# Kernel tuning notes

Hardware: AMD Instinct MI355X
Metric: run time of the kernel (lower is better)

## Reference

```python
import jax, jax.numpy as jnp
import numpy as np

B, S, D_IN, D_OUT, H = 4, 2048, 1024, 1024, 16
HD = D_OUT // H  # 64


def setup_inputs() -> dict:
    key = jax.random.key(0)
    ks = jax.random.split(key, 6)
    s = 1.0 / np.sqrt(D_IN)
    return {
        "x": jax.random.normal(ks[0], (B, S, D_IN), dtype=jnp.float32),
        "Wq": jax.random.uniform(ks[1], (D_IN, D_OUT), jnp.float32, -s, s),
        "Wk": jax.random.uniform(ks[2], (D_IN, D_OUT), jnp.float32, -s, s),
        "Wv": jax.random.uniform(ks[3], (D_IN, D_OUT), jnp.float32, -s, s),
        "Wo": jax.random.uniform(ks[4], (D_OUT, D_OUT), jnp.float32, -s, s),
        "bo": jax.random.uniform(ks[5], (D_OUT,), jnp.float32, -s, s),
    }


def reference(x, Wq, Wk, Wv, Wo, bo):
    b, s, _ = x.shape
    # QKV projections -> [b, H, s, hd]
    def split_heads(t):
        return t.reshape(b, s, H, HD).transpose(0, 2, 1, 3)
    q = split_heads(x @ Wq)
    k = split_heads(x @ Wk)
    v = split_heads(x @ Wv)
    # attention scores [b, H, s, s]
    scores = jnp.einsum("bhqd,bhkd->bhqk", q, k)
    causal = jnp.triu(jnp.ones((s, s), dtype=bool), k=1)
    scores = jnp.where(causal, -jnp.inf, scores)
    attn = jax.nn.softmax(scores / np.sqrt(HD), axis=-1)
    ctx = jnp.einsum("bhqk,bhkd->bhqd", attn, v)
    ctx = ctx.transpose(0, 2, 1, 3).reshape(b, s, D_OUT)
    return ctx @ Wo + bo
```

## Files before the change

kernel.cpp:

```cpp
#include <hip/hip_runtime.h>

typedef __attribute__((ext_vector_type(8))) short bf16x8;
typedef __attribute__((ext_vector_type(4))) float f32x4;
typedef __attribute__((ext_vector_type(4))) unsigned uint4v;

#define SM_C 0.18033688011112042f
#define MFMA16 __builtin_amdgcn_mfma_f32_16x16x32_bf16

__device__ __forceinline__ unsigned short f2bf(float f) {
  unsigned u = __builtin_bit_cast(unsigned, f);
  u += 0x7fffu + ((u >> 16) & 1u);
  return (unsigned short)(u >> 16);
}

__device__ __forceinline__ unsigned cvtpk(float lo, float hi) {
  unsigned r;
  asm volatile("v_cvt_pk_bf16_f32 %0, %1, %2" : "=v"(r) : "v"(lo), "v"(hi));
  return r;
}

__device__ __forceinline__ void gload16(const void* g, void* lds) {
  __builtin_amdgcn_global_load_lds(
      (const __attribute__((address_space(1))) void*)g,
      (__attribute__((address_space(3))) void*)lds, 16, 0, 0);
}

#define BARRIER __builtin_amdgcn_s_barrier()
#define ABARRIER asm volatile("s_barrier" ::: "memory")
#define LGKM0 asm volatile("s_waitcnt lgkmcnt(0)" ::: "memory")

__global__ __launch_bounds__(256) void cvt_x(const float* __restrict__ in,
                                             unsigned short* __restrict__ out,
                                             int n4) {
  int i = blockIdx.x * 256 + threadIdx.x;
  int stride = gridDim.x * 256;
  for (; i < n4; i += stride) {
    float4 v = ((const float4*)in)[i];
    unsigned short o0 = f2bf(v.x), o1 = f2bf(v.y), o2 = f2bf(v.z), o3 = f2bf(v.w);
    unsigned long long packed = (unsigned long long)o0 | ((unsigned long long)o1 << 16) |
                                ((unsigned long long)o2 << 32) | ((unsigned long long)o3 << 48);
    ((unsigned long long*)out)[i] = packed;
  }
}

__global__ __launch_bounds__(256) void transpose_w4(const float* __restrict__ W0,
                                                    const float* __restrict__ W1,
                                                    const float* __restrict__ W2,
                                                    const float* __restrict__ W3,
                                                    unsigned short* __restrict__ WT) {
  __shared__ float tile[32][33];
  const int z = blockIdx.z;
  const float* W = (z == 0) ? W0 : (z == 1) ? W1 : (z == 2) ? W2 : W3;
  unsigned short* WTo = WT + (size_t)z * 1048576;
  int bx = blockIdx.x, by = blockIdx.y;
  int x = bx * 32 + threadIdx.x;
  for (int i = 0; i < 4; ++i) {
    int r = threadIdx.y + i * 8;
    tile[r][threadIdx.x] = W[(by * 32 + r) * 1024 + x];
  }
  __syncthreads();
  int nx = by * 32 + threadIdx.x;
  for (int i = 0; i < 4; ++i) {
    int r = threadIdx.y + i * 8;
    WTo[(long)(bx * 32 + r) * 1024 + nx] = f2bf(tile[threadIdx.x][r]);
  }
}

__global__ __launch_bounds__(256) void transpose_v(const unsigned short* __restrict__ QKV,
                                                   unsigned short* __restrict__ Vt) {
  __shared__ alignas(16) unsigned short tile[64][74];
  const int bid = blockIdx.x;
  const int st = bid & 31, bh = bid >> 5;
  const int b = bh >> 4, h = bh & 15;
  const int t = threadIdx.x;
  const int r = t >> 2, c16 = (t & 3) * 16;
  const unsigned short* src =
      QKV + ((long)(b * 2048 + st * 64 + r)) * 3072 + 2048 + h * 64 + c16;
  uint4v v0 = *(const uint4v*)src;
  uint4v v1 = *(const uint4v*)(src + 8);
  unsigned* dst32 = (unsigned*)&tile[r][c16];
  dst32[0] = v0[0]; dst32[1] = v0[1]; dst32[2] = v0[2]; dst32[3] = v0[3];
  dst32[4] = v1[0]; dst32[5] = v1[1]; dst32[6] = v1[2]; dst32[7] = v1[3];
  __syncthreads();
  const int lw = t & 63, w = t >> 6;
  const int vp = (lw & 32) | (((lw >> 2) & 3) << 3) | (((lw >> 4) & 1) << 2) | (lw & 3);
#pragma unroll
  for (int k = 0; k < 16; ++k) {
    int hd = w * 16 + k;
    Vt[((long)(bh * 64 + hd)) * 2048 + st * 64 + vp] = tile[lw][hd];
  }
}

template <int NR, int FP32OUT>
__global__ __launch_bounds__(512, 1) void gemm3b(const unsigned short* __restrict__ A,
                                                 const unsigned short* __restrict__ BT,
                                                 unsigned short* __restrict__ Cb,
                                                 float* __restrict__ Cf,
                                                 const float* __restrict__ bias,
                                                 int M, int N, int K) {
  constexpr int BN = NR * 64;
  __shared__ alignas(16) unsigned short As[3][256 * 64];
  __shared__ alignas(16) unsigned short Bs[2][BN * 64];

  const int nbn = N / BN;
  const int tmg = (M / 256) / 8;
  const int cc = blockIdx.x >> 3, xc = blockIdx.x & 7;
  const int tm = xc * tmg + cc / nbn, tn = cc % nbn;

  const int t = threadIdx.x, l = t & 63, wid = t >> 6;
  const int wm = wid >> 2, wn = wid & 3;
  const int lr = l & 15, lg = l >> 4;

  f32x4 acc[8][NR] = {};

  const int sq = t >> 3;
  const int sslot8 = ((t & 7) ^ (sq & 7)) * 8;
  const unsigned short* Ath = A + ((long)tm * 256 + sq) * K + sslot8;
  const unsigned short* Bth = BT + ((long)tn * BN + sq) * K + sslot8;
  const int ldsoff = sq * 64 + (t & 7) * 8;

#define STGA(buf, q, kt) \
  gload16(Ath + (long)((q)*64) * K + (kt)*64, &As[buf][(q)*4096 + ldsoff])
#define STGB(buf, u, kt) \
  gload16(Bth + (long)((u)*64) * K + (kt)*64, &Bs[buf][(u)*4096 + ldsoff])

  const int NT = K >> 6;
#pragma unroll
  for (int q = 0; q < 4; ++q) STGA(0, q, 0);
#pragma unroll
  for (int u = 0; u < NR; ++u) STGB(0, u, 0);
#pragma unroll
  for (int q = 0; q < 4; ++q) STGA(1, q, 1);

  const int offk0 = (lg ^ (lr & 7)) * 8;
  const int offk1 = ((4 + lg) ^ (lr & 7)) * 8;
  const int arow0 = (wm * 128 + lr) * 64;
  const int brow0 = (wn * (NR * 16) + lr) * 64;

#define DS_A(MH)                                                   \
  _Pragma("unroll") for (int m_ = 0; m_ < 4; ++m_) {               \
    const unsigned short* ap_ = Ac + arow0 + ((MH)*4 + m_) * 1024; \
    af[m_][0] = *(const bf16x8*)(ap_ + offk0);                     \
    af[m_][1] = *(const bf16x8*)(ap_ + offk1);                     \
  }
#define DS_B_ALL                                          \
  _Pragma("unroll") for (int n_ = 0; n_ < NR; ++n_) {     \
    const unsigned short* bp_ = Bc + brow0 + n_ * 1024;   \
    bfr[n_][0] = *(const bf16x8*)(bp_ + offk0);           \
    bfr[n_][1] = *(const bf16x8*)(bp_ + offk1);           \
  }
#define MM(MH)                                                              \
  __builtin_amdgcn_s_setprio(1);                                            \
  _Pragma("unroll") for (int m_ = 0; m_ < 4; ++m_)                          \
  _Pragma("unroll") for (int n_ = 0; n_ < NR; ++n_) {                       \
    acc[(MH)*4 + m_][n_] = MFMA16(af[m_][0], bfr[n_][0],                    \
                                  acc[(MH)*4 + m_][n_], 0, 0, 0);           \
    acc[(MH)*4 + m_][n_] = MFMA16(af[m_][1], bfr[n_][1],                    \
                                  acc[(MH)*4 + m_][n_], 0, 0, 0);           \
  }                                                                         \
  __builtin_amdgcn_s_setprio(0);

  int cur3 = 0;
  int stg3 = 2;
  for (int tt = 0; tt < NT; ++tt) {
    const unsigned short* Ac = As[cur3];
    const unsigned short* Bc = Bs[tt & 1];

    bf16x8 af[4][2];
    bf16x8 bfr[NR][2];

    if (tt == NT - 1) asm volatile("s_waitcnt vmcnt(0)" ::: "memory");
    else              asm volatile("s_waitcnt vmcnt(4)" ::: "memory");
    BARRIER;
    DS_A(0);
    DS_B_ALL;
    if (tt + 1 < NT) {
      const int nbB = (tt + 1) & 1;
#pragma unroll
      for (int u = 0; u < NR; ++u) STGB(nbB, u, tt + 1);
    }
    BARRIER;
    LGKM0;
    MM(0);

    DS_A(1);
    if (tt + 2 < NT) {
#pragma unroll
      for (int q = 0; q < 4; ++q) STGA(stg3, q, tt + 2);
    }
    BARRIER;
    LGKM0;
    MM(1);

    cur3 = (cur3 == 2) ? 0 : cur3 + 1;
    stg3 = (stg3 == 2) ? 0 : stg3 + 1;
  }
#undef DS_A
#undef DS_B_ALL
#undef MM
#undef STGA
#undef STGB

  const long crow = (long)tm * 256 + wm * 128;
  const int ccol = tn * BN + wn * (NR * 16);
#pragma unroll
  for (int m = 0; m < 8; ++m)
#pragma unroll
    for (int n = 0; n < NR; ++n)
#pragma unroll
      for (int r = 0; r < 4; ++r) {
        long row = crow + m * 16 + lg * 4 + r;
        int col = ccol + n * 16 + lr;
        if (FP32OUT)
          Cf[row * N + col] = acc[m][n][r] + bias[col];
        else
          Cb[row * N + col] = f2bf(acc[m][n][r]);
      }
}

template <int TWO>
__device__ __forceinline__ void attn_tile(
    const unsigned short* __restrict__ Kc, const unsigned short* __restrict__ Vc,
    int lr, int lg, bool mask0, bool mask1, int kv0, int q0row, int q1row,
    const bf16x8 (&qf)[2][2], f32x4 (&cacc)[2][4], float (&m_r)[2], float (&l_r)[2]) {
  constexpr int S0 = TWO ? 0 : 1;
  f32x4 p[2][4];
#pragma unroll
  for (int s = S0; s < 2; ++s)
#pragma unroll
    for (int g = 0; g < 4; ++g) p[s][g] = f32x4{0.f, 0.f, 0.f, 0.f};

  __builtin_amdgcn_s_setprio(1);
#pragma unroll
  for (int g = 0; g < 4; ++g) {
    const int key = g * 16 + lr;
    const int swz = (key & 7) << 3;
#pragma unroll
    for (int c = 0; c < 2; ++c) {
      bf16x8 kf = *(const bf16x8*)(Kc + key * 64 + ((c * 32 + lg * 8) ^ swz));
#pragma unroll
      for (int s = S0; s < 2; ++s)
        p[s][g] = MFMA16(kf, qf[s][c], p[s][g], 0, 0, 0);
    }
  }
  __builtin_amdgcn_s_setprio(0);

  if (TWO && mask0) {
#pragma unroll
    for (int g = 0; g < 4; ++g)
#pragma unroll
      for (int r = 0; r < 4; ++r)
        if (kv0 + g * 16 + lg * 4 + r > q0row) p[0][g][r] = -1e30f;
  }
  if (mask1) {
#pragma unroll
    for (int g = 0; g < 4; ++g)
#pragma unroll
      for (int r = 0; r < 4; ++r)
        if (kv0 + g * 16 + lg * 4 + r > q1row) p[1][g][r] = -1e30f;
  }

  unsigned pk[2][4][2];
#pragma unroll
  for (int s = S0; s < 2; ++s) {
    float mloc = p[s][0][0];
#pragma unroll
    for (int g = 0; g < 4; ++g)
#pragma unroll
      for (int r = 0; r < 4; ++r) mloc = fmaxf(mloc, p[s][g][r]);
    mloc = fmaxf(mloc, __shfl_xor(mloc, 16));
    mloc = fmaxf(mloc, __shfl_xor(mloc, 32));
    const bool defer = __all(mloc <= m_r[s] + 44.0f);
    const float mn = defer ? m_r[s] : fmaxf(m_r[s], mloc);
    const float nmc = -mn * SM_C;
    float rs = 0.f;
#pragma unroll
    for (int g = 0; g < 4; ++g)
#pragma unroll
      for (int r = 0; r < 4; ++r) {
        float e = __builtin_amdgcn_exp2f(__builtin_fmaf(p[s][g][r], SM_C, nmc));
        p[s][g][r] = e;
        rs += e;
      }
    rs += __shfl_xor(rs, 16);
    rs += __shfl_xor(rs, 32);
    if (defer) {
      l_r[s] += rs;
    } else {
      float alpha = __builtin_amdgcn_exp2f((m_r[s] - mn) * SM_C);
      l_r[s] = l_r[s] * alpha + rs;
      m_r[s] = mn;
      float alq[4];
#pragma unroll
      for (int r = 0; r < 4; ++r) alq[r] = __shfl(alpha, lg * 20 + r);
#pragma unroll
      for (int n = 0; n < 4; ++n)
#pragma unroll
        for (int r = 0; r < 4; ++r) cacc[s][n][r] *= alq[r];
    }
#pragma unroll
    for (int g = 0; g < 4; ++g) {
      pk[s][g][0] = cvtpk(p[s][g][0], p[s][g][1]);
      pk[s][g][1] = cvtpk(p[s][g][2], p[s][g][3]);
    }
  }

#pragma unroll
  for (int sl = 0; sl < 2; ++sl) {
    bf16x8 vf[4];
#pragma unroll
    for (int n = 0; n < 4; ++n) {
      const int hd = n * 16 + lr;
      vf[n] = *(const bf16x8*)(Vc + hd * 64 + ((sl * 32 + lg * 8) ^ ((hd & 7) << 3)));
    }
    __builtin_amdgcn_s_setprio(1);
#pragma unroll
    for (int s = S0; s < 2; ++s) {
      uint4v pw = {pk[s][2 * sl][0], pk[s][2 * sl][1], pk[s][2 * sl + 1][0], pk[s][2 * sl + 1][1]};
      bf16x8 pa = __builtin_bit_cast(bf16x8, pw);
#pragma unroll
      for (int n = 0; n < 4; ++n)
        cacc[s][n] = MFMA16(pa, vf[n], cacc[s][n], 0, 0, 0);
    }
    __builtin_amdgcn_s_setprio(0);
  }
}

__global__ __launch_bounds__(256, 4) void flash_attn(const unsigned short* __restrict__ QKV,
                                                     const unsigned short* __restrict__ Vt,
                                                     unsigned short* __restrict__ Ctx) {
  __shared__ alignas(16) unsigned short Ks[2][64 * 64];
  __shared__ alignas(16) unsigned short Vs[2][64 * 64];
  const int bid = blockIdx.x;
  const int qt = bid >> 6;
  const int bh = bid & 63;
  const int b = bh >> 4, h = bh & 15;
  const int t = threadIdx.x, l = t & 63, w = t >> 6;
  const int lr = l & 15, lg = l >> 4;
  const long rowbase = (long)b * 2048;
  const int colbase = h * 64;
  const int q0 = qt * 64 + w * 16;
  const int q1 = (31 - qt) * 64 + w * 16;
  const int q0row = q0 + lr, q1row = q1 + lr;
  const int nkv = 32 - qt;

  bf16x8 qf[2][2];
#pragma unroll
  for (int c = 0; c < 2; ++c) {
    qf[0][c] = *(const bf16x8*)(QKV + (rowbase + q0 + lr) * 3072 + colbase + c * 32 + lg * 8);
    qf[1][c] = *(const bf16x8*)(QKV + (rowbase + q1 + lr) * 3072 + colbase + c * 32 + lg * 8);
  }

  f32x4 cacc[2][4];
  float m_r[2], l_r[2];
#pragma unroll
  for (int s = 0; s < 2; ++s) {
    m_r[s] = -1e30f;
    l_r[s] = 0.f;
#pragma unroll
    for (int n = 0; n < 4; ++n) cacc[s][n] = f32x4{0.f, 0.f, 0.f, 0.f};
  }

  const int srow = w * 16 + (l >> 3);
  const int scol = (l & 7) * 8;
  const int kswz = scol ^ ((srow & 7) << 3);
  const unsigned short* kp = QKV + (rowbase + srow) * 3072 + 1024 + colbase + kswz;
  const unsigned short* vp = Vt + ((long)(bh * 64 + srow)) * 2048 + kswz;
  unsigned short* ksd0 = &Ks[0][(w * 16) * 64];
  unsigned short* vsd0 = &Vs[0][(w * 16) * 64];

#define STAGE(buf)                                    \
  do {                                                \
    gload16(kp, ksd0 + (buf) * 4096);                 \
    gload16(kp + 8 * 3072, ksd0 + (buf) * 4096 + 512);\
    gload16(vp, vsd0 + (buf) * 4096);                 \
    gload16(vp + 8 * 2048, vsd0 + (buf) * 4096 + 512);\
    kp += 64 * 3072;                                  \
    vp += 64;                                         \
  } while (0)

#define TILE_WAIT(j)                                                          \
  do {                                                                        \
    if ((j) == nkv - 1) asm volatile("s_waitcnt vmcnt(0)" ::: "memory");      \
    else                asm volatile("s_waitcnt vmcnt(4)" ::: "memory");      \
    asm volatile("s_barrier" ::: "memory");                                   \
  } while (0)

  STAGE(0);
  STAGE(1);

  int j = 0;
  for (; j <= qt; ++j) {
    const int cur = j & 1;
    TILE_WAIT(j);
    attn_tile<1>(Ks[cur], Vs[cur], lr, lg, j == qt, false, j * 64, q0row, q1row,
                 qf, cacc, m_r, l_r);
    asm volatile("s_barrier" ::: "memory");
    if (j + 2 < nkv) STAGE(cur);
  }
  for (; j < nkv; ++j) {
    const int cur = j & 1;
    TILE_WAIT(j);
    attn_tile<0>(Ks[cur], Vs[cur], lr, lg, false, j == nkv - 1, j * 64, q0row, q1row,
                 qf, cacc, m_r, l_r);
    asm volatile("s_barrier" ::: "memory");
    if (j + 2 < nkv) STAGE(cur);
  }
#undef STAGE
#undef TILE_WAIT

#pragma unroll
  for (int s = 0; s < 2; ++s) {
    float invl = 1.f / l_r[s];
    float ilq[4];
#pragma unroll
    for (int r = 0; r < 4; ++r) ilq[r] = __shfl(invl, lg * 20 + r);
    const int qs = (s == 0) ? q0 : q1;
#pragma unroll
    for (int n = 0; n < 4; ++n)
#pragma unroll
      for (int r = 0; r < 4; ++r) {
        long row = rowbase + qs + lg * 4 + r;
        Ctx[row * 1024 + colbase + n * 16 + lr] = f2bf(cacc[s][n][r] * ilq[r]);
      }
  }
}

extern "C" void kernel_launch(void* const* d_in, const int* in_sizes, int n_in,
                              void* d_out, int out_size, void* d_ws, size_t ws_size,
                              hipStream_t stream) {
  (void)in_sizes; (void)n_in; (void)out_size; (void)ws_size;
  const float* x  = (const float*)d_in[0];
  const float* Wq = (const float*)d_in[1];
  const float* Wk = (const float*)d_in[2];
  const float* Wv = (const float*)d_in[3];
  const float* Wo = (const float*)d_in[4];
  const float* bo = (const float*)d_in[5];
  float* out = (float*)d_out;

  unsigned short* ws = (unsigned short*)d_ws;
  unsigned short* xb  = ws;
  unsigned short* Vt  = ws;
  unsigned short* WqT = ws + 8388608;
  unsigned short* WkT = WqT + 1048576;
  unsigned short* WvT = WkT + 1048576;
  unsigned short* WoT = WvT + 1048576;
  unsigned short* QKV = WoT + 1048576;
  unsigned short* Ctx = QKV + 25165824;

  cvt_x<<<2048, 256, 0, stream>>>(x, xb, 8192 * 1024 / 4);

  dim3 tb(32, 8), tg(32, 32, 4);
  transpose_w4<<<tg, tb, 0, stream>>>(Wq, Wk, Wv, Wo, WqT);

  gemm3b<3, 0><<<512, 512, 0, stream>>>(xb, WqT, QKV, nullptr, nullptr,
                                        8192, 3072, 1024);

  transpose_v<<<2048, 256, 0, stream>>>(QKV, Vt);

  flash_attn<<<1024, 256, 0, stream>>>(QKV, Vt, Ctx);

  gemm3b<2, 1><<<256, 512, 0, stream>>>(Ctx, WoT, nullptr, out, bo,
                                        8192, 1024, 1024);
}
```

Measured before the change: 159.3 us.

## Fuse V transpose into QKV GEMM epilogue and pack softmax math

The QKV GEMM epilogue now writes Q and K into separate contiguous planes and writes V directly in the permuted transposed layout used by attention. This removes the separate transpose_v kernel and its extra read and write of V. The GEMM tile width is reduced from NR=3 to NR=2 with more blocks so that each tile column maps onto exactly one plane. The attention softmax is also rewritten to use packed fp32 FMA, add and mul instructions. The V epilogue now issues scattered 8-byte stores, and the smaller tile lowers per-block reuse in the GEMM.

```diff
diff --git a/kernel.cpp b/kernel.cpp
--- a/kernel.cpp
+++ b/kernel.cpp
@@ -2,6 +2,7 @@
 
 typedef __attribute__((ext_vector_type(8))) short bf16x8;
 typedef __attribute__((ext_vector_type(4))) float f32x4;
+typedef __attribute__((ext_vector_type(2))) float f32x2;
 typedef __attribute__((ext_vector_type(4))) unsigned uint4v;
 
 #define SM_C 0.18033688011112042f
@@ -19,6 +20,22 @@
   return r;
 }
 
+__device__ __forceinline__ f32x2 pk_fma(f32x2 a, f32x2 b, f32x2 c) {
+  f32x2 d;
+  asm("v_pk_fma_f32 %0, %1, %2, %3" : "=v"(d) : "v"(a), "v"(b), "v"(c));
+  return d;
+}
+__device__ __forceinline__ f32x2 pk_add(f32x2 a, f32x2 b) {
+  f32x2 d;
+  asm("v_pk_add_f32 %0, %1, %2" : "=v"(d) : "v"(a), "v"(b));
+  return d;
+}
+__device__ __forceinline__ f32x2 pk_mul(f32x2 a, f32x2 b) {
+  f32x2 d;
+  asm("v_pk_mul_f32 %0, %1, %2" : "=v"(d) : "v"(a), "v"(b));
+  return d;
+}
+
 __device__ __forceinline__ void gload16(const void* g, void* lds) {
   __builtin_amdgcn_global_load_lds(
       (const __attribute__((address_space(1))) void*)g,
@@ -26,7 +43,6 @@
 }
 
 #define BARRIER __builtin_amdgcn_s_barrier()
-#define ABARRIER asm volatile("s_barrier" ::: "memory")
 #define LGKM0 asm volatile("s_waitcnt lgkmcnt(0)" ::: "memory")
 
 __global__ __launch_bounds__(256) void cvt_x(const float* __restrict__ in,
@@ -66,32 +82,7 @@
   }
 }
 
-__global__ __launch_bounds__(256) void transpose_v(const unsigned short* __restrict__ QKV,
-                                                   unsigned short* __restrict__ Vt) {
-  __shared__ alignas(16) unsigned short tile[64][74];
-  const int bid = blockIdx.x;
-  const int st = bid & 31, bh = bid >> 5;
-  const int b = bh >> 4, h = bh & 15;
-  const int t = threadIdx.x;
-  const int r = t >> 2, c16 = (t & 3) * 16;
-  const unsigned short* src =
-      QKV + ((long)(b * 2048 + st * 64 + r)) * 3072 + 2048 + h * 64 + c16;
-  uint4v v0 = *(const uint4v*)src;
-  uint4v v1 = *(const uint4v*)(src + 8);
-  unsigned* dst32 = (unsigned*)&tile[r][c16];
-  dst32[0] = v0[0]; dst32[1] = v0[1]; dst32[2] = v0[2]; dst32[3] = v0[3];
-  dst32[4] = v1[0]; dst32[5] = v1[1]; dst32[6] = v1[2]; dst32[7] = v1[3];
-  __syncthreads();
-  const int lw = t & 63, w = t >> 6;
-  const int vp = (lw & 32) | (((lw >> 2) & 3) << 3) | (((lw >> 4) & 1) << 2) | (lw & 3);
-#pragma unroll
-  for (int k = 0; k < 16; ++k) {
-    int hd = w * 16 + k;
-    Vt[((long)(bh * 64 + hd)) * 2048 + st * 64 + vp] = tile[lw][hd];
-  }
-}
-
-template <int NR, int FP32OUT>
+template <int NR, int MODE>
 __global__ __launch_bounds__(512, 1) void gemm3b(const unsigned short* __restrict__ A,
                                                  const unsigned short* __restrict__ BT,
                                                  unsigned short* __restrict__ Cb,
@@ -203,19 +194,54 @@
 
   const long crow = (long)tm * 256 + wm * 128;
   const int ccol = tn * BN + wn * (NR * 16);
-#pragma unroll
-  for (int m = 0; m < 8; ++m)
-#pragma unroll
-    for (int n = 0; n < NR; ++n)
-#pragma unroll
-      for (int r = 0; r < 4; ++r) {
-        long row = crow + m * 16 + lg * 4 + r;
-        int col = ccol + n * 16 + lr;
-        if (FP32OUT)
+
+  if constexpr (MODE == 1) {
+#pragma unroll
+    for (int m = 0; m < 8; ++m)
+#pragma unroll
+      for (int n = 0; n < NR; ++n)
+#pragma unroll
+        for (int r = 0; r < 4; ++r) {
+          long row = crow + m * 16 + lg * 4 + r;
+          int col = ccol + n * 16 + lr;
           Cf[row * N + col] = acc[m][n][r] + bias[col];
-        else
-          Cb[row * N + col] = f2bf(acc[m][n][r]);
+        }
+  } else {
+    if (tn < 16) {
+      unsigned short* plane = Cb + ((tn < 8) ? 0 : 8388608);
+      const int pc = ccol - ((tn < 8) ? 0 : 1024);
+#pragma unroll
+      for (int m = 0; m < 8; ++m)
+#pragma unroll
+        for (int n = 0; n < NR; ++n)
+#pragma unroll
+          for (int r = 0; r < 4; ++r) {
+            long row = crow + m * 16 + lg * 4 + r;
+            plane[row * 1024 + pc + n * 16 + lr] = f2bf(acc[m][n][r]);
+          }
+    } else {
+      unsigned short* VtW = Cb + 16777216;
+      const int bq = (tm >> 3) << 4;
+      const int sbase = (tm & 7) * 256 + wm * 128;
+#pragma unroll
+      for (int m = 0; m < 8; ++m) {
+        const int lwb = (m * 16 + lg * 4) & 63;
+        const int stt = (sbase + m * 16 + lg * 4) >> 6;
+        const int vp0 = (lwb & 32) | (((lwb >> 2) & 3) << 3) | (((lwb >> 4) & 1) << 2);
+#pragma unroll
+        for (int n = 0; n < NR; ++n) {
+          const int vcol = ccol + n * 16 + lr - 2048;
+          const long vtrow = (long)(bq + (vcol >> 6)) * 64 + (vcol & 63);
+          unsigned long long pk4 =
+              (unsigned long long)f2bf(acc[m][n][0]) |
+              ((unsigned long long)f2bf(acc[m][n][1]) << 16) |
+              ((unsigned long long)f2bf(acc[m][n][2]) << 32) |
+              ((unsigned long long)f2bf(acc[m][n][3]) << 48);
+          *(unsigned long long*)(VtW + vtrow * 2048 + stt * 64 + vp0) = pk4;
+        }
       }
+    }
+  }
 }
 
 template <int TWO>
@@ -260,6 +286,7 @@
         if (kv0 + g * 16 + lg * 4 + r > q1row) p[1][g][r] = -1e30f;
   }
 
+  const f32x2 C2 = {SM_C, SM_C};
   unsigned pk[2][4][2];
 #pragma unroll
   for (int s = S0; s < 2; ++s) {
@@ -272,16 +299,28 @@
     mloc = fmaxf(mloc, __shfl_xor(mloc, 32));
     const bool defer = __all(mloc <= m_r[s] + 44.0f);
     const float mn = defer ? m_r[s] : fmaxf(m_r[s], mloc);
-    const float nmc = -mn * SM_C;
-    float rs = 0.f;
-#pragma unroll
-    for (int g = 0; g < 4; ++g)
-#pragma unroll
-      for (int r = 0; r < 4; ++r) {
-        float e = __builtin_amdgcn_exp2f(__builtin_fmaf(p[s][g][r], SM_C, nmc));
-        p[s][g][r] = e;
-        rs += e;
-      }
+    f32x2 nmc2;
+    nmc2[0] = nmc2[1] = -mn * SM_C;
+    f32x2 ex[4][2];
+#pragma unroll
+    for (int g = 0; g < 4; ++g) {
+      f32x2 lo = {p[s][g][0], p[s][g][1]};
+      f32x2 hi = {p[s][g][2], p[s][g][3]};
+      ex[g][0] = pk_fma(lo, C2, nmc2);
+      ex[g][1] = pk_fma(hi, C2, nmc2);
+      ex[g][0][0] = __builtin_amdgcn_exp2f(ex[g][0][0]);
+      ex[g][0][1] = __builtin_amdgcn_exp2f(ex[g][0][1]);
+      ex[g][1][0] = __builtin_amdgcn_exp2f(ex[g][1][0]);
+      ex[g][1][1] = __builtin_amdgcn_exp2f(ex[g][1][1]);
+    }
+    f32x2 r0 = pk_add(ex[0][0], ex[0][1]);
+    f32x2 r1 = pk_add(ex[1][0], ex[1][1]);
+    f32x2 r2 = pk_add(ex[2][0], ex[2][1]);
+    f32x2 r3 = pk_add(ex[3][0], ex[3][1]);
+    f32x2 r01 = pk_add(r0, r1);
+    f32x2 r23 = pk_add(r2, r3);
+    f32x2 rv = pk_add(r01, r23);
+    float rs = rv[0] + rv[1];
     rs += __shfl_xor(rs, 16);
     rs += __shfl_xor(rs, 32);
     if (defer) {
@@ -293,15 +332,22 @@
       float alq[4];
 #pragma unroll
       for (int r = 0; r < 4; ++r) alq[r] = __shfl(alpha, lg * 20 + r);
-#pragma unroll
-      for (int n = 0; n < 4; ++n)
-#pragma unroll
-        for (int r = 0; r < 4; ++r) cacc[s][n][r] *= alq[r];
+      f32x2 alo = {alq[0], alq[1]};
+      f32x2 ahi = {alq[2], alq[3]};
+#pragma unroll
+      for (int n = 0; n < 4; ++n) {
+        f32x2 clo = {cacc[s][n][0], cacc[s][n][1]};
+        f32x2 chi = {cacc[s][n][2], cacc[s][n][3]};
+        clo = pk_mul(clo, alo);
+        chi = pk_mul(chi, ahi);
+        cacc[s][n][0] = clo[0]; cacc[s][n][1] = clo[1];
+        cacc[s][n][2] = chi[0]; cacc[s][n][3] = chi[1];
+      }
     }
 #pragma unroll
     for (int g = 0; g < 4; ++g) {
-      pk[s][g][0] = cvtpk(p[s][g][0], p[s][g][1]);
-      pk[s][g][1] = cvtpk(p[s][g][2], p[s][g][3]);
+      pk[s][g][0] = cvtpk(ex[g][0][0], ex[g][0][1]);
+      pk[s][g][1] = cvtpk(ex[g][1][0], ex[g][1][1]);
     }
   }
 
@@ -326,7 +372,8 @@
   }
 }
 
-__global__ __launch_bounds__(256, 4) void flash_attn(const unsigned short* __restrict__ QKV,
+__global__ __launch_bounds__(256, 4) void flash_attn(const unsigned short* __restrict__ Qp,
+                                                     const unsigned short* __restrict__ Kp,
                                                      const unsigned short* __restrict__ Vt,
                                                      unsigned short* __restrict__ Ctx) {
   __shared__ alignas(16) unsigned short Ks[2][64 * 64];
@@ -347,8 +394,8 @@
   bf16x8 qf[2][2];
 #pragma unroll
   for (int c = 0; c < 2; ++c) {
-    qf[0][c] = *(const bf16x8*)(QKV + (rowbase + q0 + lr) * 3072 + colbase + c * 32 + lg * 8);
-    qf[1][c] = *(const bf16x8*)(QKV + (rowbase + q1 + lr) * 3072 + colbase + c * 32 + lg * 8);
+    qf[0][c] = *(const bf16x8*)(Qp + (rowbase + q0 + lr) * 1024 + colbase + c * 32 + lg * 8);
+    qf[1][c] = *(const bf16x8*)(Qp + (rowbase + q1 + lr) * 1024 + colbase + c * 32 + lg * 8);
   }
 
   f32x4 cacc[2][4];
@@ -364,7 +411,7 @@
   const int srow = w * 16 + (l >> 3);
   const int scol = (l & 7) * 8;
   const int kswz = scol ^ ((srow & 7) << 3);
-  const unsigned short* kp = QKV + (rowbase + srow) * 3072 + 1024 + colbase + kswz;
+  const unsigned short* kp = Kp + (rowbase + srow) * 1024 + colbase + kswz;
   const unsigned short* vp = Vt + ((long)(bh * 64 + srow)) * 2048 + kswz;
   unsigned short* ksd0 = &Ks[0][(w * 16) * 64];
   unsigned short* vsd0 = &Vs[0][(w * 16) * 64];
@@ -372,10 +419,10 @@
 #define STAGE(buf)                                    \
   do {                                                \
     gload16(kp, ksd0 + (buf) * 4096);                 \
-    gload16(kp + 8 * 3072, ksd0 + (buf) * 4096 + 512);\
+    gload16(kp + 8 * 1024, ksd0 + (buf) * 4096 + 512);\
     gload16(vp, vsd0 + (buf) * 4096);                 \
     gload16(vp + 8 * 2048, vsd0 + (buf) * 4096 + 512);\
-    kp += 64 * 3072;                                  \
+    kp += 64 * 1024;                                  \
     vp += 64;                                         \
   } while (0)
 
@@ -440,12 +487,12 @@
 
   unsigned short* ws = (unsigned short*)d_ws;
   unsigned short* xb  = ws;
-  unsigned short* Vt  = ws;
   unsigned short* WqT = ws + 8388608;
-  unsigned short* WkT = WqT + 1048576;
-  unsigned short* WvT = WkT + 1048576;
-  unsigned short* WoT = WvT + 1048576;
-  unsigned short* QKV = WoT + 1048576;
+  unsigned short* WoT = WqT + 3145728;
+  unsigned short* QKV = WqT + 4194304;
+  unsigned short* Qp  = QKV;
+  unsigned short* Kp  = QKV + 8388608;
+  unsigned short* Vt  = QKV + 16777216;
   unsigned short* Ctx = QKV + 25165824;
 
   cvt_x<<<2048, 256, 0, stream>>>(x, xb, 8192 * 1024 / 4);
@@ -453,12 +500,10 @@
   dim3 tb(32, 8), tg(32, 32, 4);
   transpose_w4<<<tg, tb, 0, stream>>>(Wq, Wk, Wv, Wo, WqT);
 
-  gemm3b<3, 0><<<512, 512, 0, stream>>>(xb, WqT, QKV, nullptr, nullptr,
+  gemm3b<2, 0><<<768, 512, 0, stream>>>(xb, WqT, QKV, nullptr, nullptr,
                                         8192, 3072, 1024);
 
-  transpose_v<<<2048, 256, 0, stream>>>(QKV, Vt);
-
-  flash_attn<<<1024, 256, 0, stream>>>(QKV, Vt, Ctx);
+  flash_attn<<<1024, 256, 0, stream>>>(Qp, Kp, Vt, Ctx);
 
   gemm3b<2, 1><<<256, 512, 0, stream>>>(Ctx, WoT, nullptr, out, bo,
                                         8192, 1024, 1024);
```

Measured after the change: 156.9 us. Within noise of the previous version (-1.5%).
